# Optimization experiments

Measured on AMD Instinct MI355X. Metric: run time of the kernel, lower is better.

The kernel has to match this reference:

```python
import jax, jax.numpy as jnp
import numpy as np


def setup_inputs() -> dict:
    key = jax.random.key(0)
    k1, k2 = jax.random.split(key)
    x = jax.random.normal(k1, (32, 256, 128, 128), dtype=jnp.float32)
    conv_w = jax.random.normal(k2, (1, 2, 3, 3), dtype=jnp.float32) * 0.1
    return {"x": x, "conv_w": conv_w}


def reference(x, conv_w):
    # channel-wise mean and max -> [B,1,H,W] each
    avg_out = jnp.mean(x, axis=1, keepdims=True)
    max_out = jnp.max(x, axis=1, keepdims=True)
    cat = jnp.concatenate([avg_out, max_out], axis=1)  # [B,2,H,W]
    # 3x3 conv, 2->1 channels, padding=1, no bias (NCHW, OIHW)
    y = jax.lax.conv_general_dilated(
        cat, conv_w,
        window_strides=(1, 1),
        padding=((1, 1), (1, 1)),
        dimension_numbers=("NCHW", "OIHW", "NCHW"),
    )  # [B,1,H,W]
    # note: original returns conv_out * sigmoid(conv_out) (SiLU of conv output)
    return y * jax.nn.sigmoid(y)
```

## Files before the change

kernel.cpp:

```cpp
#include <hip/hip_runtime.h>

#define BATCH 32
#define CH    256
#define HH    128
#define WW    128
#define HW    (HH * WW)
#define HW4   (HW / 4)

typedef float f32x4 __attribute__((ext_vector_type(4)));

__global__ __launch_bounds__(256) void reduce_mean_max(
    const float* __restrict__ x, float* __restrict__ red) {
    int idx = blockIdx.x * blockDim.x + threadIdx.x;
    int b  = idx >> 12;
    int p4 = idx & (HW4 - 1);

    const f32x4* xp = reinterpret_cast<const f32x4*>(x)
                      + (size_t)b * (size_t)CH * HW4 + p4;

    f32x4 s = {0.f, 0.f, 0.f, 0.f};
    f32x4 m = {-INFINITY, -INFINITY, -INFINITY, -INFINITY};
    #pragma unroll 16
    for (int c = 0; c < CH; ++c) {
        f32x4 t = __builtin_nontemporal_load(xp + (size_t)c * HW4);
        s += t;
        m.x = fmaxf(m.x, t.x);
        m.y = fmaxf(m.y, t.y);
        m.z = fmaxf(m.z, t.z);
        m.w = fmaxf(m.w, t.w);
    }

    const float inv = 1.0f / (float)CH;
    f32x4 avg = s * inv;

    f32x4* rp = reinterpret_cast<f32x4*>(red) + (size_t)b * (2 * HW4) + p4;
    rp[0]   = avg;
    rp[HW4] = m;
}

#define TROWS 8
#define LW    (WW + 2)

__global__ __launch_bounds__(256) void conv3x3_silu(
    const float* __restrict__ red, const float* __restrict__ cw,
    float* __restrict__ out) {
    __shared__ float lin[2][TROWS + 2][LW];

    int blk = blockIdx.x;
    int b   = blk >> 4;
    int r0  = (blk & 15) * TROWS;
    int tid = threadIdx.x;

    if (tid < 2 * (TROWS + 2)) {
        int ch  = tid / (TROWS + 2);
        int row = tid - ch * (TROWS + 2);
        lin[ch][row][0]      = 0.f;
        lin[ch][row][LW - 1] = 0.f;
    }

    const float4* red4 = reinterpret_cast<const float4*>(red);
    for (int l = tid; l < 640; l += 256) {
        int ch  = l / 320;
        int rem = l - ch * 320;
        int row = rem >> 5;
        int c4  = rem & 31;
        int gr  = r0 - 1 + row;
        float4 v = make_float4(0.f, 0.f, 0.f, 0.f);
        if (gr >= 0 && gr < HH)
            v = red4[((size_t)b * 2 + ch) * HW4 + gr * 32 + c4];
        float* dst = &lin[ch][row][1 + 4 * c4];
        dst[0] = v.x; dst[1] = v.y; dst[2] = v.z; dst[3] = v.w;
    }

    float wg[18];
    #pragma unroll
    for (int i = 0; i < 18; ++i) wg[i] = cw[i];

    __syncthreads();

    int lr = tid >> 5;
    int w0 = (tid & 31) * 4;

    float acc[4] = {0.f, 0.f, 0.f, 0.f};
    #pragma unroll
    for (int ch = 0; ch < 2; ++ch) {
        #pragma unroll
        for (int dr = 0; dr < 3; ++dr) {
            const float* rowp = &lin[ch][lr + dr][w0];
            float e[6];
            #pragma unroll
            for (int k = 0; k < 6; ++k) e[k] = rowp[k];
            const float* wp = &wg[ch * 9 + dr * 3];
            #pragma unroll
            for (int j = 0; j < 4; ++j)
                acc[j] += e[j] * wp[0] + e[j + 1] * wp[1] + e[j + 2] * wp[2];
        }
    }

    float4 o;
    o.x = acc[0] / (1.f + expf(-acc[0]));
    o.y = acc[1] / (1.f + expf(-acc[1]));
    o.z = acc[2] / (1.f + expf(-acc[2]));
    o.w = acc[3] / (1.f + expf(-acc[3]));
    reinterpret_cast<float4*>(out)[(size_t)b * HW4 + (r0 + lr) * 32 + (w0 >> 2)] = o;
}

extern "C" void kernel_launch(void* const* d_in, const int* in_sizes, int n_in,
                              void* d_out, int out_size, void* d_ws, size_t ws_size,
                              hipStream_t stream) {
    const float* x  = (const float*)d_in[0];
    const float* cw = (const float*)d_in[1];
    float* out = (float*)d_out;
    float* red = (float*)d_ws;

    reduce_mean_max<<<(BATCH * HW4) / 256, 256, 0, stream>>>(x, red);
    conv3x3_silu<<<BATCH * (HH / TROWS), 256, 0, stream>>>(red, cw, out);
}
```

Before: 94.29 us.

## Fuse channel reduction and conv into one cooperative kernel with grid sync

Merges the mean/max reduction and the 3x3 conv+SiLU into a single cooperative kernel. Each block keeps its own reduced rows in shared memory and only fetches the two halo rows from global memory after a grid-wide sync. This removes one kernel launch and most of the reread of the reduced map. The cost is a grid barrier and a launch that only works if all 512 blocks can be resident at once.

```diff
diff --git a/kernel.cpp b/kernel.cpp
--- a/kernel.cpp
+++ b/kernel.cpp
@@ -1,4 +1,7 @@
 #include <hip/hip_runtime.h>
+#include <hip/hip_cooperative_groups.h>
+
+namespace cg = cooperative_groups;
 
 #define BATCH 32
 #define CH    256
@@ -6,18 +9,33 @@
 #define WW    128
 #define HW    (HH * WW)
 #define HW4   (HW / 4)
+#define TROWS 8
+#define LW    (WW + 2)
 
 typedef float f32x4 __attribute__((ext_vector_type(4)));
 
-__global__ __launch_bounds__(256) void reduce_mean_max(
-    const float* __restrict__ x, float* __restrict__ red) {
-    int idx = blockIdx.x * blockDim.x + threadIdx.x;
-    int b  = idx >> 12;
-    int p4 = idx & (HW4 - 1);
+__global__ __launch_bounds__(256) void fused_sam(
+    const float* __restrict__ x, const float* __restrict__ cw,
+    float* __restrict__ red, float* __restrict__ out) {
+    __shared__ float lin[2][TROWS + 2][LW];
+
+    int blk = blockIdx.x;
+    int b   = blk >> 4;
+    int r0  = (blk & 15) * TROWS;
+    int tid = threadIdx.x;
+    int lr  = tid >> 5;
+    int c4  = tid & 31;
+    int p4  = r0 * 32 + tid;
+
+    if (tid < 2 * (TROWS + 2)) {
+        int ch  = tid / (TROWS + 2);
+        int row = tid - ch * (TROWS + 2);
+        lin[ch][row][0]      = 0.f;
+        lin[ch][row][LW - 1] = 0.f;
+    }
 
     const f32x4* xp = reinterpret_cast<const f32x4*>(x)
                       + (size_t)b * (size_t)CH * HW4 + p4;
-
     f32x4 s = {0.f, 0.f, 0.f, 0.f};
     f32x4 m = {-INFINITY, -INFINITY, -INFINITY, -INFINITY};
     #pragma unroll 16
@@ -29,58 +47,39 @@
         m.z = fmaxf(m.z, t.z);
         m.w = fmaxf(m.w, t.w);
     }
-
-    const float inv = 1.0f / (float)CH;
-    f32x4 avg = s * inv;
+    f32x4 avg = s * (1.0f / (float)CH);
 
     f32x4* rp = reinterpret_cast<f32x4*>(red) + (size_t)b * (2 * HW4) + p4;
     rp[0]   = avg;
     rp[HW4] = m;
-}
 
-#define TROWS 8
-#define LW    (WW + 2)
-
-__global__ __launch_bounds__(256) void conv3x3_silu(
-    const float* __restrict__ red, const float* __restrict__ cw,
-    float* __restrict__ out) {
-    __shared__ float lin[2][TROWS + 2][LW];
-
-    int blk = blockIdx.x;
-    int b   = blk >> 4;
-    int r0  = (blk & 15) * TROWS;
-    int tid = threadIdx.x;
-
-    if (tid < 2 * (TROWS + 2)) {
-        int ch  = tid / (TROWS + 2);
-        int row = tid - ch * (TROWS + 2);
-        lin[ch][row][0]      = 0.f;
-        lin[ch][row][LW - 1] = 0.f;
-    }
-
-    const float4* red4 = reinterpret_cast<const float4*>(red);
-    for (int l = tid; l < 640; l += 256) {
-        int ch  = l / 320;
-        int rem = l - ch * 320;
-        int row = rem >> 5;
-        int c4  = rem & 31;
-        int gr  = r0 - 1 + row;
-        float4 v = make_float4(0.f, 0.f, 0.f, 0.f);
-        if (gr >= 0 && gr < HH)
-            v = red4[((size_t)b * 2 + ch) * HW4 + gr * 32 + c4];
-        float* dst = &lin[ch][row][1 + 4 * c4];
-        dst[0] = v.x; dst[1] = v.y; dst[2] = v.z; dst[3] = v.w;
-    }
+    float* da = &lin[0][1 + lr][1 + 4 * c4];
+    da[0] = avg.x; da[1] = avg.y; da[2] = avg.z; da[3] = avg.w;
+    float* dm = &lin[1][1 + lr][1 + 4 * c4];
+    dm[0] = m.x;  dm[1] = m.y;  dm[2] = m.z;  dm[3] = m.w;
 
     float wg[18];
     #pragma unroll
     for (int i = 0; i < 18; ++i) wg[i] = cw[i];
 
+    cg::this_grid().sync();
+
+    const f32x4* red4 = reinterpret_cast<const f32x4*>(red);
+    if (tid < 128) {
+        int which = tid >> 6;
+        int ch    = (tid >> 5) & 1;
+        int cc    = tid & 31;
+        int gr    = which ? (r0 + TROWS) : (r0 - 1);
+        int lrow  = which ? (TROWS + 1) : 0;
+        f32x4 v = {0.f, 0.f, 0.f, 0.f};
+        if (gr >= 0 && gr < HH)
+            v = red4[((size_t)b * 2 + ch) * HW4 + gr * 32 + cc];
+        float* dst = &lin[ch][lrow][1 + 4 * cc];
+        dst[0] = v.x; dst[1] = v.y; dst[2] = v.z; dst[3] = v.w;
+    }
     __syncthreads();
 
-    int lr = tid >> 5;
-    int w0 = (tid & 31) * 4;
-
+    int w0 = 4 * c4;
     float acc[4] = {0.f, 0.f, 0.f, 0.f};
     #pragma unroll
     for (int ch = 0; ch < 2; ++ch) {
@@ -102,7 +101,7 @@
     o.y = acc[1] / (1.f + expf(-acc[1]));
     o.z = acc[2] / (1.f + expf(-acc[2]));
     o.w = acc[3] / (1.f + expf(-acc[3]));
-    reinterpret_cast<float4*>(out)[(size_t)b * HW4 + (r0 + lr) * 32 + (w0 >> 2)] = o;
+    reinterpret_cast<float4*>(out)[(size_t)b * HW4 + (r0 + lr) * 32 + c4] = o;
 }
 
 extern "C" void kernel_launch(void* const* d_in, const int* in_sizes, int n_in,
@@ -113,6 +112,7 @@
     float* out = (float*)d_out;
     float* red = (float*)d_ws;
 
-    reduce_mean_max<<<(BATCH * HW4) / 256, 256, 0, stream>>>(x, red);
-    conv3x3_silu<<<BATCH * (HH / TROWS), 256, 0, stream>>>(red, cw, out);
+    void* args[] = {(void*)&x, (void*)&cw, (void*)&red, (void*)&out};
+    hipLaunchCooperativeKernel((void*)fused_sam, dim3(BATCH * (HH / TROWS)),
+                               dim3(256), args, 0, stream);
 }
```

Result: slower. 160.0 us (+69.7%).
